# Kernel optimization log

Measured on AMD Instinct MI355X. Metric: run time of the kernel, lower is better.

Reference implementation:

```python
import jax, jax.numpy as jnp
import numpy as np

N_NODES = 100000
N_EDGES = 3200000
IN_DIM = 128
OUT_DIM = 128


def setup_inputs() -> dict:
    key = jax.random.key(0)
    k1, k2, k3, k4, k5 = jax.random.split(key, 5)
    features = jax.random.normal(k1, (N_NODES, IN_DIM), dtype=jnp.float32)
    edge_src = jax.random.randint(k2, (N_EDGES,), 0, N_NODES, dtype=jnp.int32)
    edge_dst = jax.random.randint(k3, (N_EDGES,), 0, N_NODES, dtype=jnp.int32)
    edge_vals = jax.random.uniform(k4, (N_EDGES,), dtype=jnp.float32)
    # kaiming_normal_ on [in, out] with fan_in = in
    weight = jax.random.normal(k5, (IN_DIM, OUT_DIM), dtype=jnp.float32) * np.sqrt(2.0 / IN_DIM)
    bias = jnp.zeros((OUT_DIM,), dtype=jnp.float32)
    return {
        "features": features,
        "edge_src": edge_src,
        "edge_dst": edge_dst,
        "edge_vals": edge_vals,
        "weight": weight,
        "bias": bias,
    }


def reference(features, edge_src, edge_dst, edge_vals, weight, bias):
    # h = X @ W  : [N, out]
    h = features @ weight
    # SpMM: out[dst] += A[dst, src] * h[src]   (COO edge-list aggregation)
    msgs = h[edge_src] * edge_vals[:, None]          # [E, out]
    agg = jax.ops.segment_sum(msgs, edge_dst, num_segments=N_NODES)
    return agg + bias
```

## Files before the change

### kernel.cpp

```cpp
#include <hip/hip_runtime.h>

#define IN_DIM 128
#define OUT_DIM 128
#define BIN_SHIFT 7
#define BIN_NODES 128
#define NBIN_MAX 800
#define NPART 8
#define CAPX 1024
#define CAP_LDS 4864
#define TILE_A 3072
#define NR 8
#define NKEY (BIN_NODES * NR)

typedef __attribute__((ext_vector_type(8))) short bf16x8;
typedef __attribute__((ext_vector_type(4))) float f32x4;
typedef __attribute__((ext_vector_type(2))) float f32x2;

__device__ inline unsigned short f2bf(float f) {
    unsigned u = __float_as_uint(f);
    unsigned r = (u + 0x7fff + ((u >> 16) & 1)) >> 16;
    return (unsigned short)r;
}
__device__ inline float bflo(unsigned h) { return __uint_as_float(h << 16); }
__device__ inline float bfhi(unsigned h) { return __uint_as_float(h & 0xffff0000u); }

__global__ __launch_bounds__(256) void pack_w_zero(const float* __restrict__ W,
                                                   unsigned short* __restrict__ Wpack,
                                                   int* __restrict__ gcur, int nbin8) {
    int idx = blockIdx.x * 256 + threadIdx.x;
    if (idx < nbin8) gcur[idx] = 0;
    if (idx >= 16384) return;
    int j = idx & 7;
    int lane = (idx >> 3) & 63;
    int kc = (idx >> 9) & 3;
    int tn = idx >> 11;
    int k = kc * 32 + (lane >> 4) * 8 + j;
    int n = tn * 16 + (lane & 15);
    Wpack[idx] = f2bf(W[k * OUT_DIM + n]);
}

struct BinSmem {
    int2 eL[TILE_A];
    int hist[NBIN_MAX];
    int s0[NBIN_MAX];
    int s1[NBIN_MAX];
    unsigned short bL[TILE_A];
    unsigned short idx[TILE_A];
    unsigned short bS[TILE_A];
};

__global__ __launch_bounds__(256) void phase1(
    const int* __restrict__ src, const int* __restrict__ dst,
    const float* __restrict__ vals, int* __restrict__ gcur,
    int2* __restrict__ entries, int n_edges, int nbin, int nA,
    const float* __restrict__ X, const unsigned short* __restrict__ Wpack,
    unsigned short* __restrict__ Hb, int n_rows, int nG) {
    __shared__ BinSmem sm;

    int b = blockIdx.x;
    int isGemm, widx;
    if (b < 2 * nG) {
        isGemm = (b & 1) == 0;
        widx = b >> 1;
    } else {
        isGemm = 0;
        widx = nG + (b - 2 * nG);
    }

    const int tid = threadIdx.x;

    if (!isGemm) {
        const int part = widx & (NPART - 1);
        const int base = widx * TILE_A;
        const int n0 = n_edges - base;
        if (n0 <= 0) return;
        const int n = (n0 < TILE_A) ? n0 : TILE_A;

        for (int i = tid; i < nbin; i += 256) sm.hist[i] = 0;
        __syncthreads();

        for (int i = tid; i < n; i += 256) {
            int d = dst[base + i];
            int s = src[base + i];
            float v = vals[base + i];
            int bin = d >> BIN_SHIFT;
            sm.eL[i] = make_int2(s | ((d & (BIN_NODES - 1)) << 17), __float_as_int(v));
            sm.bL[i] = (unsigned short)bin;
            atomicAdd(&sm.hist[bin], 1);
        }
        __syncthreads();

        for (int l = tid; l < nbin; l += 256) sm.s0[l] = sm.hist[l];
        __syncthreads();
        int* sin = sm.s0;
        int* sout = sm.s1;
        for (int dd = 1; dd < nbin; dd <<= 1) {
            for (int l = tid; l < nbin; l += 256)
                sout[l] = sin[l] + ((l >= dd) ? sin[l - dd] : 0);
            __syncthreads();
            int* t = sin; sin = sout; sout = t;
        }

        for (int l = tid; l < nbin; l += 256) {
            int c = sm.hist[l];
            int ex = sin[l] - c;
            int g = (c > 0) ? atomicAdd(&gcur[part * nbin + l], c) : 0;
            sout[l] = g - ex;
            sm.hist[l] = ex;
        }
        __syncthreads();

        for (int i = tid; i < n; i += 256) {
            int bb = sm.bL[i];
            int p = atomicAdd(&sm.hist[bb], 1);
            sm.idx[p] = (unsigned short)i;
            sm.bS[p] = (unsigned short)bb;
        }
        __syncthreads();

        for (int p = tid; p < n; p += 256) {
            int bb = sm.bS[p];
            int gp = sout[bb] + p;
            if (gp < CAPX)
                entries[((long long)(part * nbin + bb)) * CAPX + gp] = sm.eL[sm.idx[p]];
        }
        return;
    }

    int strip = widx * 4 + (tid >> 6);
    long long m0 = (long long)strip * 32;
    if (m0 >= n_rows) return;
    int lane = tid & 63;
    int quad = lane >> 4;
    int low = lane & 15;

    const bf16x8* B = (const bf16x8*)Wpack;

    long long r0 = m0 + low;
    long long r1 = m0 + 16 + low;
    if (r1 >= n_rows) r1 = n_rows - 1;
    if (r0 >= n_rows) r0 = n_rows - 1;

    f32x4 acc[2][8] = {};

#pragma unroll
    for (int kc = 0; kc < 4; ++kc) {
        const float4* p0 = (const float4*)(X + r0 * IN_DIM + kc * 32 + quad * 8);
        const float4* p1 = (const float4*)(X + r1 * IN_DIM + kc * 32 + quad * 8);
        float4 x0a = p0[0], x0b = p0[1];
        float4 x1a = p1[0], x1b = p1[1];
        bf16x8 afr0, afr1;
        afr0[0] = f2bf(x0a.x); afr0[1] = f2bf(x0a.y); afr0[2] = f2bf(x0a.z); afr0[3] = f2bf(x0a.w);
        afr0[4] = f2bf(x0b.x); afr0[5] = f2bf(x0b.y); afr0[6] = f2bf(x0b.z); afr0[7] = f2bf(x0b.w);
        afr1[0] = f2bf(x1a.x); afr1[1] = f2bf(x1a.y); afr1[2] = f2bf(x1a.z); afr1[3] = f2bf(x1a.w);
        afr1[4] = f2bf(x1b.x); afr1[5] = f2bf(x1b.y); afr1[6] = f2bf(x1b.z); afr1[7] = f2bf(x1b.w);
#pragma unroll
        for (int tn = 0; tn < 8; ++tn) {
            bf16x8 bfr = B[(tn * 4 + kc) * 64 + lane];
            acc[0][tn] = __builtin_amdgcn_mfma_f32_16x16x32_bf16(afr0, bfr, acc[0][tn], 0, 0, 0);
            acc[1][tn] = __builtin_amdgcn_mfma_f32_16x16x32_bf16(afr1, bfr, acc[1][tn], 0, 0, 0);
        }
    }

#pragma unroll
    for (int t = 0; t < 2; ++t) {
#pragma unroll
        for (int tn = 0; tn < 8; ++tn) {
#pragma unroll
            for (int r = 0; r < 4; ++r) {
                long long row = m0 + t * 16 + quad * 4 + r;
                if (row < n_rows) {
                    int col = tn * 16 + low;
                    Hb[row * OUT_DIM + col] = f2bf(acc[t][tn][r]);
                }
            }
        }
    }
}

__global__ __launch_bounds__(1024) void binB_gather(
    const int2* __restrict__ entries, const int* __restrict__ gcur,
    const unsigned short* __restrict__ Hb, const float* __restrict__ bias,
    float* __restrict__ out, int n_nodes, int nbin) {
    __shared__ int2 ent[CAP_LDS];
    __shared__ int hist[NKEY];
    __shared__ int dbase[NKEY];
    __shared__ int cur[NKEY];

    const int bin = blockIdx.x;
    const int tid = threadIdx.x;

    int scnt[NPART], sbase_[NPART];
    int tot = 0;
#pragma unroll
    for (int s = 0; s < NPART; ++s) {
        int c = gcur[s * nbin + bin];
        scnt[s] = (c < CAPX) ? c : CAPX;
        sbase_[s] = tot;
        tot += scnt[s];
    }

    hist[tid] = 0;
    __syncthreads();

    const unsigned rdiv = (unsigned)((n_nodes + NR - 1) / NR);
    int2 e[NPART];
    int key[NPART];
    bool ok[NPART];
#pragma unroll
    for (int s = 0; s < NPART; ++s) {
        ok[s] = (tid < scnt[s]) && (sbase_[s] + tid < CAP_LDS);
        if (ok[s]) e[s] = entries[((long long)(s * nbin + bin)) * CAPX + tid];
    }
#pragma unroll
    for (int s = 0; s < NPART; ++s)
        if (ok[s]) {
            int ld = (e[s].x >> 17) & (BIN_NODES - 1);
            int rg = (int)((unsigned)(e[s].x & 0x1ffff) / rdiv);
            key[s] = ld * NR + rg;
            atomicAdd(&hist[key[s]], 1);
        }
    __syncthreads();

    dbase[tid] = hist[tid];
    __syncthreads();
    for (int d = 1; d < NKEY; d <<= 1) {
        int v = (tid >= d) ? dbase[tid - d] : 0;
        __syncthreads();
        dbase[tid] += v;
        __syncthreads();
    }
    {
        int ex = dbase[tid] - hist[tid];
        __syncthreads();
        dbase[tid] = ex;
        cur[tid] = ex;
    }
    __syncthreads();

#pragma unroll
    for (int s = 0; s < NPART; ++s)
        if (ok[s]) {
            int pos = atomicAdd(&cur[key[s]], 1);
            ent[pos] = e[s];
        }
    __syncthreads();

    const int wave = tid >> 6;
    const int lane = tid & 63;
    const unsigned short* hrow = Hb + lane * 2;
    float2 bb = ((const float2*)bias)[lane];

    f32x2 acc[8];
#pragma unroll
    for (int k = 0; k < 8; ++k) { acc[k][0] = bb.x; acc[k][1] = bb.y; }

    for (int r = 0; r < NR; ++r) {
#pragma unroll
        for (int k = 0; k < 8; ++k) {
            const int kk = (wave * 8 + k) * NR + r;
            const int beg = dbase[kk];
            const int end = beg + hist[kk];
            for (int i = beg; i < end; i += 8) {
                unsigned h[8];
                float v[8];
                bool okj[8];
#pragma unroll
                for (int j = 0; j < 8; ++j) {
                    okj[j] = (i + j < end);
                    if (okj[j]) {
                        int2 c = ent[i + j];
                        v[j] = __int_as_float(c.y);
                        h[j] = *(const unsigned*)(hrow + (long long)(c.x & 0x1ffff) * OUT_DIM);
                    }
                }
#pragma unroll
                for (int j = 0; j < 8; ++j)
                    if (okj[j]) {
                        f32x2 hv; hv[0] = bflo(h[j]); hv[1] = bfhi(h[j]);
                        f32x2 vv; vv[0] = v[j]; vv[1] = v[j];
                        acc[k] += vv * hv;
                    }
            }
        }
        __syncthreads();
    }

    const int node0 = bin * BIN_NODES + wave * 8;
#pragma unroll
    for (int k = 0; k < 8; ++k) {
        int node = node0 + k;
        if (node < n_nodes) {
            float2 res; res.x = acc[k][0]; res.y = acc[k][1];
            ((float2*)(out + (long long)node * OUT_DIM))[lane] = res;
        }
    }
}

extern "C" void kernel_launch(void* const* d_in, const int* in_sizes, int n_in,
                              void* d_out, int out_size, void* d_ws, size_t ws_size,
                              hipStream_t stream) {
    const float* features  = (const float*)d_in[0];
    const int* edge_src    = (const int*)d_in[1];
    const int* edge_dst    = (const int*)d_in[2];
    const float* edge_vals = (const float*)d_in[3];
    const float* weight    = (const float*)d_in[4];
    const float* bias      = (const float*)d_in[5];

    const int n_nodes = in_sizes[0] / IN_DIM;
    const int n_edges = in_sizes[1];
    const int nbin = (n_nodes + BIN_NODES - 1) / BIN_NODES;

    int2* entries       = (int2*)d_ws;
    unsigned short* Hb  = (unsigned short*)(entries + (long long)NPART * nbin * CAPX);
    unsigned short* Wp  = Hb + (long long)n_nodes * OUT_DIM;
    int* gcur           = (int*)(Wp + 16384);

    float* out = (float*)d_out;

    pack_w_zero<<<64, 256, 0, stream>>>(weight, Wp, gcur, NPART * nbin);

    const int nA = (n_edges + TILE_A - 1) / TILE_A;
    const int n_strips = (n_nodes + 31) / 32;
    const int nG = (n_strips + 3) / 4;
    phase1<<<nA + nG, 256, 0, stream>>>(edge_src, edge_dst, edge_vals, gcur,
                                        entries, n_edges, nbin, nA,
                                        features, Wp, Hb, n_nodes, nG);

    binB_gather<<<nbin, 1024, 0, stream>>>(entries, gcur, Hb, bias, out, n_nodes, nbin);
}
```

Baseline: 337.4 us.

## Accumulate per-node sums in LDS and merge each wave's 8 node segments

Reorders the sort key so each wave's 8 destination nodes within a source-range form one contiguous edge segment. The wave now walks that whole segment with full 8-wide unrolled gather batches, accumulating into a 64KB LDS accumulator indexed by local node rather than per-node registers. This is meant to cut the tail and branch overhead of many short per-node loops and raise memory-level parallelism. In exchange it adds LDS read-modify-write traffic and raises LDS use, which may limit occupancy. The bias add and the store are moved to a coalesced float4 pass over the LDS accumulator.

```diff
diff --git a/kernel.cpp b/kernel.cpp
--- a/kernel.cpp
+++ b/kernel.cpp
@@ -182,6 +182,7 @@
     const int2* __restrict__ entries, const int* __restrict__ gcur,
     const unsigned short* __restrict__ Hb, const float* __restrict__ bias,
     float* __restrict__ out, int n_nodes, int nbin) {
+    __shared__ float accS[BIN_NODES * 128];
     __shared__ int2 ent[CAP_LDS];
     __shared__ int hist[NKEY];
     __shared__ int dbase[NKEY];
@@ -200,6 +201,7 @@
         tot += scnt[s];
     }
 
+    for (int i = tid; i < BIN_NODES * 128; i += 1024) accS[i] = 0.f;
     hist[tid] = 0;
     __syncthreads();
 
@@ -217,7 +219,7 @@
         if (ok[s]) {
             int ld = (e[s].x >> 17) & (BIN_NODES - 1);
             int rg = (int)((unsigned)(e[s].x & 0x1ffff) / rdiv);
-            key[s] = ld * NR + rg;
+            key[s] = rg * BIN_NODES + ld;
             atomicAdd(&hist[key[s]], 1);
         }
     __syncthreads();
@@ -249,51 +251,62 @@
     const int wave = tid >> 6;
     const int lane = tid & 63;
     const unsigned short* hrow = Hb + lane * 2;
-    float2 bb = ((const float2*)bias)[lane];
-
-    f32x2 acc[8];
-#pragma unroll
-    for (int k = 0; k < 8; ++k) { acc[k][0] = bb.x; acc[k][1] = bb.y; }
+    float* alane = accS + lane * 2;
 
     for (int r = 0; r < NR; ++r) {
-#pragma unroll
-        for (int k = 0; k < 8; ++k) {
-            const int kk = (wave * 8 + k) * NR + r;
-            const int beg = dbase[kk];
-            const int end = beg + hist[kk];
-            for (int i = beg; i < end; i += 8) {
-                unsigned h[8];
-                float v[8];
-                bool okj[8];
-#pragma unroll
-                for (int j = 0; j < 8; ++j) {
-                    okj[j] = (i + j < end);
-                    if (okj[j]) {
-                        int2 c = ent[i + j];
-                        v[j] = __int_as_float(c.y);
-                        h[j] = *(const unsigned*)(hrow + (long long)(c.x & 0x1ffff) * OUT_DIM);
-                    }
-                }
-#pragma unroll
-                for (int j = 0; j < 8; ++j)
-                    if (okj[j]) {
-                        f32x2 hv; hv[0] = bflo(h[j]); hv[1] = bfhi(h[j]);
-                        f32x2 vv; vv[0] = v[j]; vv[1] = v[j];
-                        acc[k] += vv * hv;
-                    }
+        const int k0 = r * BIN_NODES + wave * 8;
+        const int beg = dbase[k0];
+        const int end = dbase[k0 + 7] + hist[k0 + 7];
+
+        int i = beg;
+        for (; i + 8 <= end; i += 8) {
+            unsigned h[8];
+            float v[8];
+            int ld[8];
+#pragma unroll
+            for (int j = 0; j < 8; ++j) {
+                int2 c = ent[i + j];
+                v[j] = __int_as_float(c.y);
+                ld[j] = (c.x >> 17) & (BIN_NODES - 1);
+                h[j] = *(const unsigned*)(hrow + (c.x & 0x1ffff) * OUT_DIM);
             }
-        }
-        __syncthreads();
-    }
-
-    const int node0 = bin * BIN_NODES + wave * 8;
-#pragma unroll
-    for (int k = 0; k < 8; ++k) {
-        int node = node0 + k;
-        if (node < n_nodes) {
-            float2 res; res.x = acc[k][0]; res.y = acc[k][1];
-            ((float2*)(out + (long long)node * OUT_DIM))[lane] = res;
-        }
+#pragma unroll
+            for (int j = 0; j < 8; ++j) {
+                float* a = alane + ld[j] * 128;
+                float2 cr = *(float2*)a;
+                cr.x += v[j] * bflo(h[j]);
+                cr.y += v[j] * bfhi(h[j]);
+                *(float2*)a = cr;
+            }
+        }
+        for (; i < end; ++i) {
+            int2 c = ent[i];
+            float v = __int_as_float(c.y);
+            int ld = (c.x >> 17) & (BIN_NODES - 1);
+            unsigned h = *(const unsigned*)(hrow + (c.x & 0x1ffff) * OUT_DIM);
+            float* a = alane + ld * 128;
+            float2 cr = *(float2*)a;
+            cr.x += v * bflo(h);
+            cr.y += v * bfhi(h);
+            *(float2*)a = cr;
+        }
+        __syncthreads();
+    }
+
+    const int node0 = bin * BIN_NODES;
+    for (int f = tid; f < BIN_NODES * 32; f += 1024) {
+        int nl = f >> 5;
+        int c4 = f & 31;
+        int node = node0 + nl;
+        if (node >= n_nodes) continue;
+        float4 a = *(float4*)&accS[nl * 128 + c4 * 4];
+        float4 bq = ((const float4*)bias)[c4];
+        float4 rr;
+        rr.x = a.x + bq.x;
+        rr.y = a.y + bq.y;
+        rr.z = a.z + bq.z;
+        rr.w = a.w + bq.w;
+        *(float4*)(out + (long long)node * OUT_DIM + c4 * 4) = rr;
     }
 }
 
```

After: 346.4 us. 2.7% more time.
